# Kernel optimization log

Measured on AMD Instinct MI355X. Metric: run time of the kernel, lower is better.

Reference implementation:

```python
import jax, jax.numpy as jnp
import numpy as np

B, N = 4, 2048
VD, CD = 256, 64
H = 4
INNER = VD  # inner_ratio = 1
D = INNER // H  # head_dim = 64
EPS = 1e-5
RMS_EPS = 1e-6


def layer_norm(x, g, b):
    m = jnp.mean(x, axis=-1, keepdims=True)
    v = jnp.mean((x - m) ** 2, axis=-1, keepdims=True)
    return (x - m) * jax.lax.rsqrt(v + EPS) * g + b


def rms_norm(x, s):
    ms = jnp.mean(x * x, axis=-1, keepdims=True)
    return x * jax.lax.rsqrt(ms + RMS_EPS) * s


def split_heads(x):  # (b, n, h*d) -> (b, h, n, d)
    b, n, _ = x.shape
    return x.reshape(b, n, H, D).transpose(0, 2, 1, 3)


def setup_inputs() -> dict:
    key = jax.random.key(0)
    ks = jax.random.split(key, 10)
    w = lambda k, shp: jax.random.normal(k, shp, dtype=jnp.float32) * 0.02
    return {
        "V": jax.random.normal(ks[0], (B, N, VD), dtype=jnp.float32),
        "C": jax.random.normal(ks[1], (B, N, CD), dtype=jnp.float32),
        "vn_g": jnp.ones((VD,), jnp.float32), "vn_b": jnp.zeros((VD,), jnp.float32),
        "cn_g": jnp.ones((CD,), jnp.float32), "cn_b": jnp.zeros((CD,), jnp.float32),
        "W_vqk": w(ks[2], (VD, 2 * INNER)), "b_vqk": jnp.zeros((2 * INNER,), jnp.float32),
        "rms_v": jnp.ones((2 * INNER,), jnp.float32),
        "W_cqk": w(ks[3], (CD, 2 * INNER)), "b_cqk": jnp.zeros((2 * INNER,), jnp.float32),
        "rms_c": jnp.ones((2 * INNER,), jnp.float32),
        "W_vv": w(ks[4], (VD, INNER)), "b_vv": jnp.zeros((INNER,), jnp.float32),
        "W_cv": w(ks[5], (CD, INNER)), "b_cv": jnp.zeros((INNER,), jnp.float32),
        "W_ov": w(ks[6], (INNER, VD)), "b_ov": jnp.zeros((VD,), jnp.float32),
        "W_oc": w(ks[7], (INNER, CD)), "b_oc": jnp.zeros((CD,), jnp.float32),
    }


def reference(V, C, vn_g, vn_b, cn_g, cn_b, W_vqk, b_vqk, rms_v, W_cqk, b_cqk, rms_c,
              W_vv, b_vv, W_cv, b_cv, W_ov, b_ov, W_oc, b_oc):
    Vn = layer_norm(V, vn_g, vn_b)
    Cn = layer_norm(C, cn_g, cn_b)
    qkv = rms_norm(Vn @ W_vqk + b_vqk, rms_v)
    qkc = rms_norm(Cn @ W_cqk + b_cqk, rms_c)
    qv, kv = jnp.split(qkv, 2, axis=-1)
    qc, kc = jnp.split(qkc, 2, axis=-1)
    vv = Vn @ W_vv + b_vv
    vc = Cn @ W_cv + b_cv
    qv, kv, vv, qc, kc, vc = map(split_heads, (qv, kv, vv, qc, kc, vc))
    # shared attention map: softmax((QvKv^T + QcKc^T)/sqrt(d))
    scores = (jnp.einsum("bhnd,bhmd->bhnm", qv, kv)
              + jnp.einsum("bhnd,bhmd->bhnm", qc, kc)) / np.sqrt(D).astype(np.float32)
    attn = jax.nn.softmax(scores, axis=-1)
    out_v = jnp.einsum("bhnm,bhmd->bhnd", attn, vv).transpose(0, 2, 1, 3).reshape(B, N, INNER)
    out_c = jnp.einsum("bhnm,bhmd->bhnd", attn, vc).transpose(0, 2, 1, 3).reshape(B, N, INNER)
    return out_v @ W_ov + b_ov, out_c @ W_oc + b_oc
```

## Files before the change

### kernel.cpp

```cpp
#include <hip/hip_runtime.h>

typedef unsigned short u16;
typedef unsigned int   u32;
typedef short s16x8 __attribute__((ext_vector_type(8)));
typedef float f32x4 __attribute__((ext_vector_type(4)));

#define WS_STATSV 0
#define WS_STATSC 65536
#define WS_WT_VQK 131072
#define WS_WT_CQK 393216
#define WS_WT_VV  458752
#define WS_WT_CV  589824
#define WS_WT_OV  622592
#define WS_WT_OC  753664
#define WS_Q      786432
#define WS_K      9175040
#define WS_VT     17563648
#define WS_OV     25952256
#define WS_OC     30146560

__device__ __forceinline__ float bf2f(u16 h){
  union { u32 u; float f; } x; x.u = ((u32)h) << 16; return x.f;
}
__device__ __forceinline__ u16 f2bf(float f){
  union { float f; u32 u; } x; x.f = f;
  u32 u = x.u; u += 0x7fffu + ((u >> 16) & 1u);
  return (u16)(u >> 16);
}
__device__ __forceinline__ f32x4 mfma16(s16x8 a, s16x8 b, f32x4 c){
  return __builtin_amdgcn_mfma_f32_16x16x32_bf16(a, b, c, 0, 0, 0);
}
__device__ __forceinline__ void async16(const u16* g, u16* l){
  __builtin_amdgcn_global_load_lds(
      (const __attribute__((address_space(1))) u32*)(const void*)g,
      (__attribute__((address_space(3))) u32*)(void*)l, 16, 0, 0);
}

__global__ __launch_bounds__(256) void k_prep(const float* V, const float* C,
    const float* Wvqk, const float* Wcqk, const float* Wvv, const float* Wcv,
    const float* Wov, const float* Woc, char* ws){
  int bid = blockIdx.x;
  if (bid < 4096){
    int wid = threadIdx.x >> 6, lane = threadIdx.x & 63;
    float2* sV = (float2*)(ws + WS_STATSV);
    float2* sC = (float2*)(ws + WS_STATSC);
    float s = 0.f, s2 = 0.f; int row; float2* dst; float invn;
    if (bid < 2048){
      row = bid*4 + wid;
      const float4* p = (const float4*)(V + row*256);
      float4 v = p[lane];
      s = v.x+v.y+v.z+v.w; s2 = v.x*v.x+v.y*v.y+v.z*v.z+v.w*v.w;
      dst = sV; invn = 1.0f/256.0f;
    } else {
      row = (bid-2048)*4 + wid;
      float x = C[row*64 + lane];
      s = x; s2 = x*x;
      dst = sC; invn = 1.0f/64.0f;
    }
    for (int d=1; d<64; d<<=1){ s += __shfl_xor(s,d); s2 += __shfl_xor(s2,d); }
    if (lane == 0){
      float m = s*invn; float var = s2*invn - m*m; if (var < 0.f) var = 0.f;
      float rstd = rsqrtf(var + 1e-5f);
      float2 o; o.x = rstd; o.y = -m*rstd;
      dst[row] = o;
    }
  } else {
    int tb = bid - 4096;
    const float* src; u16* dst; int K, N, rel;
    if      (tb <  64){ src=Wvqk; dst=(u16*)(ws+WS_WT_VQK); K=256; N=512; rel=tb;     }
    else if (tb <  80){ src=Wcqk; dst=(u16*)(ws+WS_WT_CQK); K=64;  N=512; rel=tb-64;  }
    else if (tb < 112){ src=Wvv;  dst=(u16*)(ws+WS_WT_VV);  K=256; N=256; rel=tb-80;  }
    else if (tb < 120){ src=Wcv;  dst=(u16*)(ws+WS_WT_CV);  K=64;  N=256; rel=tb-112; }
    else if (tb < 152){ src=Wov;  dst=(u16*)(ws+WS_WT_OV);  K=256; N=256; rel=tb-120; }
    else              { src=Woc;  dst=(u16*)(ws+WS_WT_OC);  K=256; N=64;  rel=tb-152; }
    int e = rel*2048 + threadIdx.x*8;
    int k = e / N, n0 = e % N;
    float4 t0 = *(const float4*)(src + e);
    float4 t1 = *(const float4*)(src + e + 4);
    dst[(n0+0)*K + k] = f2bf(t0.x);
    dst[(n0+1)*K + k] = f2bf(t0.y);
    dst[(n0+2)*K + k] = f2bf(t0.z);
    dst[(n0+3)*K + k] = f2bf(t0.w);
    dst[(n0+4)*K + k] = f2bf(t1.x);
    dst[(n0+5)*K + k] = f2bf(t1.y);
    dst[(n0+6)*K + k] = f2bf(t1.z);
    dst[(n0+7)*K + k] = f2bf(t1.w);
  }
}

__device__ __forceinline__ s16x8 ln_frag(const float* A, const float* g, const float* bb,
                                         int base, int k0, float2 stt){
  float4 x0 = *(const float4*)(A + base + k0);
  float4 x1 = *(const float4*)(A + base + k0 + 4);
  float4 g0 = *(const float4*)(g + k0);
  float4 g1 = *(const float4*)(g + k0 + 4);
  float4 b0 = *(const float4*)(bb + k0);
  float4 b1 = *(const float4*)(bb + k0 + 4);
  s16x8 af;
  af[0] = (short)f2bf(fmaf(fmaf(x0.x, stt.x, stt.y), g0.x, b0.x));
  af[1] = (short)f2bf(fmaf(fmaf(x0.y, stt.x, stt.y), g0.y, b0.y));
  af[2] = (short)f2bf(fmaf(fmaf(x0.z, stt.x, stt.y), g0.z, b0.z));
  af[3] = (short)f2bf(fmaf(fmaf(x0.w, stt.x, stt.y), g0.w, b0.w));
  af[4] = (short)f2bf(fmaf(fmaf(x1.x, stt.x, stt.y), g1.x, b1.x));
  af[5] = (short)f2bf(fmaf(fmaf(x1.y, stt.x, stt.y), g1.y, b1.y));
  af[6] = (short)f2bf(fmaf(fmaf(x1.z, stt.x, stt.y), g1.z, b1.z));
  af[7] = (short)f2bf(fmaf(fmaf(x1.w, stt.x, stt.y), g1.w, b1.w));
  return af;
}

__global__ __launch_bounds__(256) void k_proj(const float* V, const float* C,
    const float* vg, const float* vb, const float* cgam, const float* cbet,
    const float* bvqk, const float* bcqk, const float* rmsv, const float* rmsc,
    const float* bvv, const float* bcv, char* ws){
  __shared__ float ssl[4][16];
  int bid = blockIdx.x;
  int tid = threadIdx.x, lane = tid & 63, w = tid >> 6;
  int c = lane & 15, q = lane >> 4;

  if (bid < 1024){
    bool csd = bid >= 512;
    int rb = (bid & 511) * 16;
    const float* A   = csd ? C : V;
    int K            = csd ? 64 : 256;
    const float2* st = (const float2*)(ws + (csd ? WS_STATSC : WS_STATSV));
    const float* g   = csd ? cgam : vg;
    const float* bb  = csd ? cbet : vb;
    const u16* Wt    = (const u16*)(ws + (csd ? WS_WT_CQK : WS_WT_VQK));
    const float* bias= csd ? bcqk : bvqk;
    const float* rms = csd ? rmsc : rmsv;
    int dOff         = csd ? 64 : 0;

    int row = rb + c;
    float2 stt = st[row];
    int j0 = w * 128;

    f32x4 acc[8];
    #pragma unroll
    for (int f=0; f<8; f++){ f32x4 z = {0.f,0.f,0.f,0.f}; acc[f] = z; }

    int nkc = K >> 5;
    for (int kc=0; kc<nkc; kc++){
      int k0 = kc*32 + q*8;
      s16x8 af = ln_frag(A, g, bb, row*K, k0, stt);
      #pragma unroll
      for (int f=0; f<8; f++){
        s16x8 bfr = *(const s16x8*)(Wt + (j0 + f*16 + c)*K + k0);
        acc[f] = mfma16(af, bfr, acc[f]);
      }
    }

    float ss[4] = {0.f,0.f,0.f,0.f};
    float rsv[8];
    #pragma unroll
    for (int f=0; f<8; f++){
      int j = j0 + f*16 + c;
      float bsv = bias[j]; rsv[f] = rms[j];
      #pragma unroll
      for (int i=0;i<4;i++){ acc[f][i] += bsv; ss[i] += acc[f][i]*acc[f][i]; }
    }
    #pragma unroll
    for (int d=1; d<16; d<<=1){
      #pragma unroll
      for (int i=0;i<4;i++) ss[i] += __shfl_xor(ss[i], d);
    }
    if (c == 0){
      #pragma unroll
      for (int i=0;i<4;i++) ssl[w][q*4 + i] = ss[i];
    }
    __syncthreads();
    float rmsr[4];
    #pragma unroll
    for (int i=0;i<4;i++){
      int rl = q*4 + i;
      float tot = ssl[0][rl] + ssl[1][rl] + ssl[2][rl] + ssl[3][rl];
      rmsr[i] = rsqrtf(tot * (1.0f/512.0f) + 1e-6f);
    }
    u16* dstb = (u16*)(ws + (w < 2 ? WS_Q : WS_K));
    float qs = (w < 2) ? 0.125f*1.44269504f : 1.0f;
    #pragma unroll
    for (int f=0; f<8; f++){
      int jj = (j0 + f*16 + c) & 255;
      int head = jj >> 6, dd = (jj & 63) + dOff;
      #pragma unroll
      for (int i=0;i<4;i++){
        int r = rb + q*4 + i;
        int b_ = r >> 11, n = r & 2047;
        dstb[((b_*4 + head)*2048 + n)*128 + dd] = f2bf(acc[f][i]*rmsr[i]*rsv[f]*qs);
      }
    }
  } else {
    int vb2 = bid - 1024;
    bool csd = vb2 >= 256;
    int rb = (vb2 & 255) * 32;
    const float* A   = csd ? C : V;
    int K            = csd ? 64 : 256;
    const float2* st = (const float2*)(ws + (csd ? WS_STATSC : WS_STATSV));
    const float* g   = csd ? cgam : vg;
    const float* bb  = csd ? cbet : vb;
    const u16* Wt    = (const u16*)(ws + (csd ? WS_WT_CV : WS_WT_VV));
    const float* bias= csd ? bcv : bvv;
    int dOff         = csd ? 64 : 0;

    int s = w & 1, cgp = w >> 1;
    int r0 = rb + s*16, row = r0 + c;
    float2 stt = st[row];
    int j0 = cgp * 128;

    f32x4 acc[8];
    #pragma unroll
    for (int f=0; f<8; f++){ f32x4 z = {0.f,0.f,0.f,0.f}; acc[f] = z; }

    int nkc = K >> 5;
    for (int kc=0; kc<nkc; kc++){
      int k0 = kc*32 + q*8;
      s16x8 af = ln_frag(A, g, bb, row*K, k0, stt);
      #pragma unroll
      for (int f=0; f<8; f++){
        s16x8 bfr = *(const s16x8*)(Wt + (j0 + f*16 + c)*K + k0);
        acc[f] = mfma16(af, bfr, acc[f]);
      }
    }
    u16* vt = (u16*)(ws + WS_VT);
    int r = r0 + q*4;
    int b_ = r >> 11, n = r & 2047;
    #pragma unroll
    for (int f=0; f<8; f++){
      int j = j0 + f*16 + c;
      float bv_ = bias[j];
      int head = j >> 6, dd = (j & 63) + dOff;
      ushort4 pk;
      pk.x = f2bf(acc[f][0] + bv_); pk.y = f2bf(acc[f][1] + bv_);
      pk.z = f2bf(acc[f][2] + bv_); pk.w = f2bf(acc[f][3] + bv_);
      *(ushort4*)(vt + ((b_*4 + head)*128 + dd)*2048 + n) = pk;
    }
  }
}

__global__ __launch_bounds__(256, 2) void k_attn(char* ws){
  const u16* Qw = (const u16*)(ws + WS_Q);
  const u16* Kw = (const u16*)(ws + WS_K);
  const u16* Vt = (const u16*)(ws + WS_VT);
  u16* Ov = (u16*)(ws + WS_OV);
  u16* Oc = (u16*)(ws + WS_OC);
  __shared__ u16 Ks[2][4096];
  __shared__ u16 Vs[2][4096];
  __shared__ u16 Ps[4][640];

  int bh = blockIdx.x & 15, qb = blockIdx.x >> 4;
  int tid = threadIdx.x, lane = tid & 63, w = tid >> 6;
  int c = lane & 15, q = lane >> 4;
  int qr0 = qb*64 + w*16;

  s16x8 qf[4];
  #pragma unroll
  for (int kc=0;kc<4;kc++)
    qf[kc] = *(const s16x8*)(Qw + (bh*2048 + qr0 + c)*128 + kc*32 + q*8);

  const u16 *ksrc0, *ksrc1, *vsrc0, *vsrc1;
  { int s0 = tid, s1 = 256 + tid;
    { int r = s0 >> 4, j = (s0 & 15) ^ (r & 15);      ksrc0 = Kw + (bh*2048 + r)*128 + j*8; }
    { int r = s1 >> 4, j = (s1 & 15) ^ (r & 15);      ksrc1 = Kw + (bh*2048 + r)*128 + j*8; }
    { int r = s0 >> 2, j = (s0 & 3) ^ ((r >> 1) & 3); vsrc0 = Vt + (bh*128 + r)*2048 + j*8; }
    { int r = s1 >> 2, j = (s1 & 3) ^ ((r >> 1) & 3); vsrc1 = Vt + (bh*128 + r)*2048 + j*8; }
  }

  f32x4 o[8];
  float lsum[4] = {0.f,0.f,0.f,0.f};
  #pragma unroll
  for (int f8=0;f8<8;f8++){ f32x4 z = {0.f,0.f,0.f,0.f}; o[f8] = z; }

  auto stage = [&](int buf, int t){
    async16(ksrc0 + t*4096, &Ks[buf][tid*8]);
    async16(ksrc1 + t*4096, &Ks[buf][(256+tid)*8]);
    async16(vsrc0 + t*32,   &Vs[buf][tid*8]);
    async16(vsrc1 + t*32,   &Vs[buf][(256+tid)*8]);
  };

  auto step = [&](int bi, int t){
    __syncthreads();
    if (t < 63) stage(bi^1, t+1);

    s16x8 kf[2][4];
    #pragma unroll
    for (int f=0;f<2;f++)
      #pragma unroll
      for (int kc=0;kc<4;kc++)
        kf[f][kc] = *(const s16x8*)(&Ks[bi][((f*16+c)*16 + (((kc*4+q) ^ c) & 15))*8]);
    s16x8 vf[8];
    #pragma unroll
    for (int f8=0;f8<8;f8++)
      vf[f8] = *(const s16x8*)(&Vs[bi][((f8*16+c)*4 + ((q ^ ((c>>1)&3)) & 3))*8]);

    f32x4 sfr[2];
    #pragma unroll
    for (int f=0;f<2;f++){ f32x4 z = {0.f,0.f,0.f,0.f}; sfr[f] = z; }
    #pragma unroll
    for (int f=0;f<2;f++)
      #pragma unroll
      for (int kc=0;kc<4;kc++)
        sfr[f] = mfma16(qf[kc], kf[f][kc], sfr[f]);

    #pragma unroll
    for (int f=0;f<2;f++){
      #pragma unroll
      for (int i=0;i<4;i++){
        float p = exp2f(sfr[f][i]);
        lsum[i] += p;
        Ps[w][(q*4 + i)*40 + f*16 + c] = f2bf(p);
      }
    }
    s16x8 pf = *(const s16x8*)(&Ps[w][c*40 + q*8]);
    #pragma unroll
    for (int f8=0;f8<8;f8++)
      o[f8] = mfma16(pf, vf[f8], o[f8]);
  };

  stage(0, 0);
  for (int t=0; t<64; t+=2){
    step(0, t);
    step(1, t+1);
  }

  #pragma unroll
  for (int d=1; d<16; d<<=1)
    #pragma unroll
    for (int i=0;i<4;i++) lsum[i] += __shfl_xor(lsum[i], d);
  float inv[4];
  #pragma unroll
  for (int i=0;i<4;i++) inv[i] = 1.0f/lsum[i];

  int b_ = bh >> 2, h = bh & 3;
  #pragma unroll
  for (int f8=0;f8<8;f8++){
    int col = f8*16 + c;
    u16* dst = (col < 64) ? Ov : Oc;
    int dd = col & 63;
    #pragma unroll
    for (int i=0;i<4;i++){
      int n = qr0 + q*4 + i;
      dst[(b_*2048 + n)*256 + h*64 + dd] = f2bf(o[f8][i]*inv[i]);
    }
  }
}

__global__ __launch_bounds__(256) void k_out(const u16* Av, const u16* Wtv, const float* bv,
                                             const u16* Ac, const u16* Wtc, const float* bc,
                                             float* out){
  int bid = blockIdx.x;
  int tid = threadIdx.x, lane = tid & 63, w = tid >> 6;
  int c = lane & 15, q = lane >> 4;
  if (bid < 512){
    int rb = bid * 16;
    int row = rb + c;
    int j0 = w * 64;
    f32x4 acc[4];
    #pragma unroll
    for (int f=0; f<4; f++){ f32x4 z = {0.f,0.f,0.f,0.f}; acc[f] = z; }
    for (int kc=0; kc<8; kc++){
      int k0 = kc*32 + q*8;
      s16x8 af = *(const s16x8*)(Av + row*256 + k0);
      #pragma unroll
      for (int f=0; f<4; f++){
        s16x8 bfr = *(const s16x8*)(Wtv + (j0 + f*16 + c)*256 + k0);
        acc[f] = mfma16(af, bfr, acc[f]);
      }
    }
    #pragma unroll
    for (int f=0; f<4; f++){
      int j = j0 + f*16 + c;
      float bb = bv[j];
      #pragma unroll
      for (int i=0;i<4;i++)
        out[(rb + q*4 + i)*256 + j] = acc[f][i] + bb;
    }
  } else {
    int rb = (bid - 512) * 64;
    int r0 = rb + w*16, row = r0 + c;
    f32x4 acc[4];
    #pragma unroll
    for (int f=0; f<4; f++){ f32x4 z = {0.f,0.f,0.f,0.f}; acc[f] = z; }
    for (int kc=0; kc<8; kc++){
      int k0 = kc*32 + q*8;
      s16x8 af = *(const s16x8*)(Ac + row*256 + k0);
      #pragma unroll
      for (int f=0; f<4; f++){
        s16x8 bfr = *(const s16x8*)(Wtc + (f*16 + c)*256 + k0);
        acc[f] = mfma16(af, bfr, acc[f]);
      }
    }
    float* oc = out + 2097152;
    #pragma unroll
    for (int f=0; f<4; f++){
      int j = f*16 + c;
      float bb = bc[j];
      #pragma unroll
      for (int i=0;i<4;i++)
        oc[(r0 + q*4 + i)*64 + j] = acc[f][i] + bb;
    }
  }
}

extern "C" void kernel_launch(void* const* d_in, const int* in_sizes, int n_in,
                              void* d_out, int out_size, void* d_ws, size_t ws_size,
                              hipStream_t stream){
  (void)in_sizes; (void)n_in; (void)out_size; (void)ws_size;
  const float* V    = (const float*)d_in[0];
  const float* C    = (const float*)d_in[1];
  const float* vng  = (const float*)d_in[2];
  const float* vnb  = (const float*)d_in[3];
  const float* cng  = (const float*)d_in[4];
  const float* cnb  = (const float*)d_in[5];
  const float* Wvqk = (const float*)d_in[6];
  const float* bvqk = (const float*)d_in[7];
  const float* rmsv = (const float*)d_in[8];
  const float* Wcqk = (const float*)d_in[9];
  const float* bcqk = (const float*)d_in[10];
  const float* rmsc = (const float*)d_in[11];
  const float* Wvv  = (const float*)d_in[12];
  const float* bvv  = (const float*)d_in[13];
  const float* Wcv  = (const float*)d_in[14];
  const float* bcv  = (const float*)d_in[15];
  const float* Wov  = (const float*)d_in[16];
  const float* bov  = (const float*)d_in[17];
  const float* Woc  = (const float*)d_in[18];
  const float* boc  = (const float*)d_in[19];
  char* ws = (char*)d_ws;
  float* out = (float*)d_out;

  k_prep<<<4256, 256, 0, stream>>>(V, C, Wvqk, Wcqk, Wvv, Wcv, Wov, Woc, ws);
  k_proj<<<1536, 256, 0, stream>>>(V, C, vng, vnb, cng, cnb,
                                   bvqk, bcqk, rmsv, rmsc, bvv, bcv, ws);
  k_attn<<<512, 256, 0, stream>>>(ws);
  k_out<<<640, 256, 0, stream>>>((const u16*)(ws + WS_OV), (const u16*)(ws + WS_WT_OV), bov,
                                 (const u16*)(ws + WS_OC), (const u16*)(ws + WS_WT_OC), boc,
                                 out);
}
```

Measured before the change: 225.7 us.

## Split attention KV range across wave pairs and give each wave two query tiles

Reorganizes the attention kernel so each wave handles 32 query rows (two 16-row tiles) instead of 16, reusing each loaded K/V fragment across two MFMA tiles. The key sequence is split into two halves processed by separate wave pairs with their own double-buffered LDS tiles, and the partial outputs and row sums are merged through shared memory at the end. This cuts LDS fragment reads per MFMA and halves the serial loop length, but raises register pressure, grows shared memory to about 74KB, and adds a final reduction step with extra barriers.

```diff
diff --git a/kernel.cpp b/kernel.cpp
--- a/kernel.cpp
+++ b/kernel.cpp
@@ -242,103 +242,161 @@
   const u16* Vt = (const u16*)(ws + WS_VT);
   u16* Ov = (u16*)(ws + WS_OV);
   u16* Oc = (u16*)(ws + WS_OC);
-  __shared__ u16 Ks[2][4096];
-  __shared__ u16 Vs[2][4096];
-  __shared__ u16 Ps[4][640];
+  __shared__ char smem[75776];
+  u16* sm16 = (u16*)smem;
 
   int bh = blockIdx.x & 15, qb = blockIdx.x >> 4;
   int tid = threadIdx.x, lane = tid & 63, w = tid >> 6;
   int c = lane & 15, q = lane >> 4;
-  int qr0 = qb*64 + w*16;
-
-  s16x8 qf[4];
+  int g = w & 1, h = w >> 1, ht = tid & 127;
+  int qr0 = qb*64 + g*32;
+
+  s16x8 qf[2][4];
   #pragma unroll
-  for (int kc=0;kc<4;kc++)
-    qf[kc] = *(const s16x8*)(Qw + (bh*2048 + qr0 + c)*128 + kc*32 + q*8);
-
-  const u16 *ksrc0, *ksrc1, *vsrc0, *vsrc1;
-  { int s0 = tid, s1 = 256 + tid;
-    { int r = s0 >> 4, j = (s0 & 15) ^ (r & 15);      ksrc0 = Kw + (bh*2048 + r)*128 + j*8; }
-    { int r = s1 >> 4, j = (s1 & 15) ^ (r & 15);      ksrc1 = Kw + (bh*2048 + r)*128 + j*8; }
-    { int r = s0 >> 2, j = (s0 & 3) ^ ((r >> 1) & 3); vsrc0 = Vt + (bh*128 + r)*2048 + j*8; }
-    { int r = s1 >> 2, j = (s1 & 3) ^ ((r >> 1) & 3); vsrc1 = Vt + (bh*128 + r)*2048 + j*8; }
-  }
-
-  f32x4 o[8];
-  float lsum[4] = {0.f,0.f,0.f,0.f};
+  for (int s=0;s<2;s++)
+    #pragma unroll
+    for (int kc=0;kc<4;kc++)
+      qf[s][kc] = *(const s16x8*)(Qw + (bh*2048 + qr0 + s*16 + c)*128 + kc*32 + q*8);
+
+  const u16* ksrc[4]; const u16* vsrc[4];
   #pragma unroll
-  for (int f8=0;f8<8;f8++){ f32x4 z = {0.f,0.f,0.f,0.f}; o[f8] = z; }
+  for (int i=0;i<4;i++){
+    int sc = i*128 + ht;
+    { int r = sc >> 4, j = (sc & 15) ^ (r & 15);
+      ksrc[i] = Kw + (bh*2048 + r)*128 + j*8; }
+    { int r = sc >> 2, j = (sc & 3) ^ ((r >> 1) & 3);
+      vsrc[i] = Vt + (bh*128 + r)*2048 + j*8; }
+  }
+
+  f32x4 o[2][8];
+  float lsum[2][4];
+  #pragma unroll
+  for (int s=0;s<2;s++){
+    #pragma unroll
+    for (int f8=0;f8<8;f8++){ f32x4 z = {0.f,0.f,0.f,0.f}; o[s][f8] = z; }
+    #pragma unroll
+    for (int i=0;i<4;i++) lsum[s][i] = 0.f;
+  }
 
   auto stage = [&](int buf, int t){
-    async16(ksrc0 + t*4096, &Ks[buf][tid*8]);
-    async16(ksrc1 + t*4096, &Ks[buf][(256+tid)*8]);
-    async16(vsrc0 + t*32,   &Vs[buf][tid*8]);
-    async16(vsrc1 + t*32,   &Vs[buf][(256+tid)*8]);
+    u16* kd = sm16 + (h*2+buf)*4096;
+    u16* vd = sm16 + 16384 + (h*2+buf)*4096;
+    #pragma unroll
+    for (int i=0;i<4;i++){
+      async16(ksrc[i] + t*4096, kd + (i*128+ht)*8);
+      async16(vsrc[i] + t*32,   vd + (i*128+ht)*8);
+    }
   };
 
-  auto step = [&](int bi, int t){
+  auto step = [&](int bi, int tt){
+    int t = h*32 + tt;
     __syncthreads();
-    if (t < 63) stage(bi^1, t+1);
-
+    if (tt < 31) stage(bi^1, t+1);
+
+    const u16* kb = sm16 + (h*2+bi)*4096;
+    const u16* vb = sm16 + 16384 + (h*2+bi)*4096;
     s16x8 kf[2][4];
     #pragma unroll
     for (int f=0;f<2;f++)
       #pragma unroll
       for (int kc=0;kc<4;kc++)
-        kf[f][kc] = *(const s16x8*)(&Ks[bi][((f*16+c)*16 + (((kc*4+q) ^ c) & 15))*8]);
+        kf[f][kc] = *(const s16x8*)(kb + ((f*16+c)*16 + (((kc*4+q) ^ c) & 15))*8);
     s16x8 vf[8];
     #pragma unroll
     for (int f8=0;f8<8;f8++)
-      vf[f8] = *(const s16x8*)(&Vs[bi][((f8*16+c)*4 + ((q ^ ((c>>1)&3)) & 3))*8]);
-
-    f32x4 sfr[2];
-    #pragma unroll
-    for (int f=0;f<2;f++){ f32x4 z = {0.f,0.f,0.f,0.f}; sfr[f] = z; }
-    #pragma unroll
-    for (int f=0;f<2;f++)
-      #pragma unroll
-      for (int kc=0;kc<4;kc++)
-        sfr[f] = mfma16(qf[kc], kf[f][kc], sfr[f]);
-
-    #pragma unroll
-    for (int f=0;f<2;f++){
-      #pragma unroll
-      for (int i=0;i<4;i++){
-        float p = exp2f(sfr[f][i]);
-        lsum[i] += p;
-        Ps[w][(q*4 + i)*40 + f*16 + c] = f2bf(p);
-      }
-    }
-    s16x8 pf = *(const s16x8*)(&Ps[w][c*40 + q*8]);
-    #pragma unroll
-    for (int f8=0;f8<8;f8++)
-      o[f8] = mfma16(pf, vf[f8], o[f8]);
+      vf[f8] = *(const s16x8*)(vb + ((f8*16+c)*4 + ((q ^ ((c>>1)&3)) & 3))*8);
+
+    f32x4 sfr[2][2];
+    #pragma unroll
+    for (int s=0;s<2;s++)
+      #pragma unroll
+      for (int f=0;f<2;f++){ f32x4 z = {0.f,0.f,0.f,0.f}; sfr[s][f] = z; }
+    #pragma unroll
+    for (int s=0;s<2;s++)
+      #pragma unroll
+      for (int f=0;f<2;f++)
+        #pragma unroll
+        for (int kc=0;kc<4;kc++)
+          sfr[s][f] = mfma16(qf[s][kc], kf[f][kc], sfr[s][f]);
+
+    #pragma unroll
+    for (int s=0;s<2;s++){
+      u16* ps = sm16 + 32768 + (w*2+s)*640;
+      #pragma unroll
+      for (int f=0;f<2;f++){
+        #pragma unroll
+        for (int i=0;i<4;i++){
+          float p = exp2f(sfr[s][f][i]);
+          lsum[s][i] += p;
+          ps[(q*4 + i)*40 + f*16 + c] = f2bf(p);
+        }
+      }
+      s16x8 pf = *(const s16x8*)(ps + c*40 + q*8);
+      #pragma unroll
+      for (int f8=0;f8<8;f8++)
+        o[s][f8] = mfma16(pf, vf[f8], o[s][f8]);
+    }
   };
 
-  stage(0, 0);
-  for (int t=0; t<64; t+=2){
-    step(0, t);
-    step(1, t+1);
-  }
-
-  #pragma unroll
-  for (int d=1; d<16; d<<=1)
-    #pragma unroll
-    for (int i=0;i<4;i++) lsum[i] += __shfl_xor(lsum[i], d);
-  float inv[4];
-  #pragma unroll
-  for (int i=0;i<4;i++) inv[i] = 1.0f/lsum[i];
-
-  int b_ = bh >> 2, h = bh & 3;
-  #pragma unroll
-  for (int f8=0;f8<8;f8++){
-    int col = f8*16 + c;
-    u16* dst = (col < 64) ? Ov : Oc;
-    int dd = col & 63;
-    #pragma unroll
-    for (int i=0;i<4;i++){
-      int n = qr0 + q*4 + i;
-      dst[(b_*2048 + n)*256 + h*64 + dd] = f2bf(o[f8][i]*inv[i]);
+  stage(0, h*32);
+  for (int tt=0; tt<32; tt+=2){
+    step(0, tt);
+    step(1, tt+1);
+  }
+
+  __syncthreads();
+  float* mg = (float*)smem;
+  if (h == 1){
+    float* d = mg + (g*64 + lane)*73;
+    #pragma unroll
+    for (int s=0;s<2;s++)
+      #pragma unroll
+      for (int f8=0;f8<8;f8++)
+        #pragma unroll
+        for (int i=0;i<4;i++) d[(s*8+f8)*4 + i] = o[s][f8][i];
+    #pragma unroll
+    for (int s=0;s<2;s++)
+      #pragma unroll
+      for (int i=0;i<4;i++) d[64 + s*4 + i] = lsum[s][i];
+  }
+  __syncthreads();
+  if (h == 0){
+    float* d = mg + (g*64 + lane)*73;
+    #pragma unroll
+    for (int s=0;s<2;s++)
+      #pragma unroll
+      for (int f8=0;f8<8;f8++)
+        #pragma unroll
+        for (int i=0;i<4;i++) o[s][f8][i] += d[(s*8+f8)*4 + i];
+    #pragma unroll
+    for (int s=0;s<2;s++)
+      #pragma unroll
+      for (int i=0;i<4;i++) lsum[s][i] += d[64 + s*4 + i];
+
+    #pragma unroll
+    for (int dd=1; dd<16; dd<<=1)
+      #pragma unroll
+      for (int s=0;s<2;s++)
+        #pragma unroll
+        for (int i=0;i<4;i++) lsum[s][i] += __shfl_xor(lsum[s][i], dd);
+
+    int b_ = bh >> 2, hh = bh & 3;
+    #pragma unroll
+    for (int s=0;s<2;s++){
+      float inv[4];
+      #pragma unroll
+      for (int i=0;i<4;i++) inv[i] = 1.0f/lsum[s][i];
+      #pragma unroll
+      for (int f8=0;f8<8;f8++){
+        int col = f8*16 + c;
+        u16* dst = (col < 64) ? Ov : Oc;
+        int ddim = col & 63;
+        #pragma unroll
+        for (int i=0;i<4;i++){
+          int n = qr0 + s*16 + q*4 + i;
+          dst[(b_*2048 + n)*256 + hh*64 + ddim] = f2bf(o[s][f8][i]*inv[i]);
+        }
+      }
     }
   }
 }
```

After: 219.3 us. -2.9%, faster.
